# Optimization experiments

Hardware: AMD Instinct MI355X
Metric: run time of the kernel (lower is better)

## Reference

```python
import jax, jax.numpy as jnp
import numpy as np

B, T, V, E, H, C = 64, 512, 30000, 256, 512, 9


def setup_inputs() -> dict:
    key = jax.random.key(0)
    ks = jax.random.split(key, 12)
    s = 0.05
    x = jax.random.randint(ks[0], (B, T), 0, V, dtype=jnp.int32)
    seq_len = jax.random.randint(ks[1], (B,), T // 2, T + 1, dtype=jnp.int32)
    y = jax.random.randint(ks[2], (B, T), 0, C, dtype=jnp.int32)
    emb = jax.random.normal(ks[3], (V, E), jnp.float32) * s
    def lstm_p(k):
        k1, k2, k3 = jax.random.split(k, 3)
        return (jax.random.normal(k1, (4 * H, E), jnp.float32) * s,
                jax.random.normal(k2, (4 * H, H), jnp.float32) * s,
                jax.random.normal(k3, (4 * H,), jnp.float32) * s)
    Wih_f, Whh_f, b_f = lstm_p(ks[4])
    Wih_b, Whh_b, b_b = lstm_p(ks[5])
    Wfc = jax.random.normal(ks[6], (C, 2 * H), jnp.float32) * s
    start_t = jax.random.normal(ks[7], (C,), jnp.float32) * 0.1
    end_t = jax.random.normal(ks[8], (C,), jnp.float32) * 0.1
    trans = jax.random.normal(ks[9], (C, C), jnp.float32) * 0.1
    return dict(x=x, seq_len=seq_len, y=y, emb=emb, Wih_f=Wih_f, Whh_f=Whh_f,
                b_f=b_f, Wih_b=Wih_b, Whh_b=Whh_b, b_b=b_b, Wfc=Wfc,
                start_t=start_t, end_t=end_t, trans=trans)


def _lstm_dir(xt, mt, Wih, Whh, b, reverse):
    # xt: [T,B,E], mt: [T,B,1] bool. State frozen at padded steps (= packed-seq semantics).
    h0 = jnp.zeros((xt.shape[1], Whh.shape[1]), xt.dtype)
    def step(carry, inp):
        h, c = carry
        x_t, m_t = inp
        g = x_t @ Wih.T + h @ Whh.T + b
        i, f, gg, o = jnp.split(g, 4, axis=-1)  # torch gate order i,f,g,o
        c_new = jax.nn.sigmoid(f) * c + jax.nn.sigmoid(i) * jnp.tanh(gg)
        h_new = jax.nn.sigmoid(o) * jnp.tanh(c_new)
        return (jnp.where(m_t, h_new, h), jnp.where(m_t, c_new, c)), h_new
    _, hs = jax.lax.scan(step, (h0, h0), (xt, mt), reverse=reverse)
    return hs  # [T,B,H]


def reference(x, seq_len, y, emb, Wih_f, Whh_f, b_f, Wih_b, Whh_b, b_b, Wfc,
              start_t, end_t, trans):
    mask = jnp.arange(T)[None, :] < seq_len[:, None]  # [B,T]
    xt = emb[x].transpose(1, 0, 2)                    # [T,B,E]
    mt = mask.T[:, :, None]
    hf = _lstm_dir(xt, mt, Wih_f, Whh_f, b_f, False)
    hb = _lstm_dir(xt, mt, Wih_b, Whh_b, b_b, True)
    out = jnp.concatenate([hf, hb], -1).transpose(1, 0, 2)  # [B,T,2H]
    out = out * mask[:, :, None]                             # pad_packed zeros
    emis = jax.nn.log_softmax(out @ Wfc.T, axis=-1)          # [B,T,C]
    maskf = mask.astype(emis.dtype)
    # --- CRF numerator (gold-path score) ---
    em_sc = jnp.take_along_axis(emis, y[..., None], -1)[..., 0] * maskf
    tr_sc = trans[y[:, :-1], y[:, 1:]] * maskf[:, 1:]
    last_tag = jnp.take_along_axis(y, (seq_len - 1)[:, None], 1)[:, 0]
    num = start_t[y[:, 0]] + em_sc.sum(-1) + tr_sc.sum(-1) + end_t[last_tag]
    # --- CRF denominator (log partition, forward algorithm) ---
    score0 = start_t[None, :] + emis[:, 0]  # [B,C]
    def step(score, inp):
        em_t, m_t = inp  # [B,C], [B]
        nxt = jax.scipy.special.logsumexp(
            score[:, :, None] + trans[None] + em_t[:, None, :], axis=1)
        return jnp.where(m_t[:, None], nxt, score), None
    score, _ = jax.lax.scan(step, score0,
                            (emis.transpose(1, 0, 2)[1:], mask.T[1:]))
    den = jax.scipy.special.logsumexp(score + end_t[None, :], axis=1)
    return -(num - den).sum()  # -sum log-likelihood
```

## Files before the change

### kernel.cpp

```cpp
#include <hip/hip_runtime.h>
#include <hip/hip_bf16.h>


using short8 = __attribute__((ext_vector_type(8))) short;
using f32x4  = __attribute__((ext_vector_type(4))) float;
using i32x4  = __attribute__((ext_vector_type(4))) int;

#define TT 512
#define BB 64

__device__ __forceinline__ unsigned short f2bf(float f) {
  unsigned int u = __builtin_bit_cast(unsigned int, f);
  u += 0x7FFFu + ((u >> 16) & 1u);
  return (unsigned short)(u >> 16);
}
__device__ __forceinline__ float bf2f(short s) {
  unsigned int u = ((unsigned int)(unsigned short)s) << 16;
  return __builtin_bit_cast(float, u);
}
__device__ __forceinline__ float fast_rcp(float x) { return __builtin_amdgcn_rcpf(x); }
__device__ __forceinline__ float sigmoid_f(float x) { return fast_rcp(1.f + __expf(-x)); }
__device__ __forceinline__ float tanh_f(float x) {
  float e = __expf(-2.f * fabsf(x));
  float r = (1.f - e) * fast_rcp(1.f + e);
  return copysignf(r, x);
}
#define SEL4(i, a0, a1, a2, a3) ((i)==0?(a0):((i)==1?(a1):((i)==2?(a2):(a3))))

__device__ __forceinline__ i32x4 load16_sc(const void* p) {
  i32x4 r;
  asm volatile("global_load_dwordx4 %0, %1, off sc0 sc1" : "=v"(r) : "v"(p));
  return r;
}
__device__ __forceinline__ i32x4 load16_sc_wait(const void* p) {
  i32x4 r;
  asm volatile("global_load_dwordx4 %0, %1, off sc0 sc1\n\ts_waitcnt vmcnt(0)"
               : "=v"(r) : "v"(p) : "memory");
  return r;
}
__device__ __forceinline__ void store16_sc(void* p, i32x4 v) {
  asm volatile("global_store_dwordx4 %0, %1, off sc0 sc1" :: "v"(p), "v"(v) : "memory");
}
#define WAITV(n) do { asm volatile("s_waitcnt vmcnt(" #n ")" ::: "memory"); \
                      __builtin_amdgcn_sched_barrier(0); } while (0)

__global__ void pack_weights(const float* __restrict__ Wih_f, const float* __restrict__ Whh_f,
                             const float* __restrict__ Wih_b, const float* __restrict__ Whh_b,
                             const float* __restrict__ Wfc,
                             short* __restrict__ WpackX, short* __restrict__ WpackH,
                             short* __restrict__ WfcPack) {
  const int bid = blockIdx.x;
  const int d = bid & 1, sl = bid >> 1;
  const float* Wih = d ? Wih_b : Wih_f;
  const float* Whh = d ? Whh_b : Whh_f;
  for (int idx = threadIdx.x; idx < 64 * 256; idx += 256) {
    int n = idx >> 8, k = idx & 255;
    int g = n & 3, jq = (n >> 2) & 3, tj = (n >> 4) & 1, nt = n >> 5;
    int r = g * 512 + sl * 16 + nt * 8 + jq * 2 + tj;
    WpackX[((size_t)bid * 64 + n) * 256 + k] = (short)f2bf(Wih[(size_t)r * 256 + k]);
  }
  for (int idx = threadIdx.x; idx < 64 * 512; idx += 256) {
    int n = idx >> 9, k = idx & 511;
    int g = n & 3, jq = (n >> 2) & 3, tj = (n >> 4) & 1, nt = n >> 5;
    int r = g * 512 + sl * 16 + nt * 8 + jq * 2 + tj;
    WpackH[((size_t)bid * 64 + n) * 512 + k] = (short)f2bf(Whh[(size_t)r * 512 + k]);
  }
  if (bid == 0) {
    for (int idx = threadIdx.x; idx < 16 * 1024; idx += 256) {
      int c = idx >> 10, k = idx & 1023;
      WfcPack[idx] = (c < 9) ? (short)f2bf(Wfc[c * 1024 + k]) : (short)0;
    }
  }
}

__global__ void pack_x(const int* __restrict__ x, const float* __restrict__ emb,
                       short* __restrict__ xpack) {
  int gid = blockIdx.x * 256 + threadIdx.x;
  int lane = gid & 63;
  int kc = (gid >> 6) & 7;
  int mt = (gid >> 9) & 3;
  int t  = gid >> 11;
  int b  = mt * 16 + (lane & 15);
  int k0 = kc * 32 + (lane >> 4) * 8;
  int vid = x[b * TT + t];
  const float* e = emb + (size_t)vid * 256 + k0;
  short8 v;
#pragma unroll
  for (int i = 0; i < 8; ++i) v[i] = (short)f2bf(e[i]);
  *reinterpret_cast<short8*>(xpack + (size_t)gid * 8) = v;
}

__global__ void init_state(int* __restrict__ flags) {
  flags[threadIdx.x] = 0;
}

__launch_bounds__(256, 1)
__global__ void lstm_step_kernel(const short8* __restrict__ xpack,
                                 const short* __restrict__ WpackX,
                                 const short* __restrict__ WpackH,
                                 short* __restrict__ hexch,
                                 int* __restrict__ flags,
                                 const float* __restrict__ b_f,
                                 const float* __restrict__ b_b,
                                 const int* __restrict__ seq_len) {
  const int bid = blockIdx.x;
  const int d = bid & 1;
  const int sl = bid >> 1;
  const int tid = threadIdx.x;
  const int wv = tid >> 6;
  const int lane = tid & 63;
  const int l15 = lane & 15;
  const int lhi = lane >> 4;
  const int q = lane & 3;
  const int jq = l15 >> 2;
  const int mtb = wv & 1;
  const int nt = wv >> 1;
  const int nbase = nt * 32;
  const int ubase = sl * 16 + nt * 8;
  const int kc_w  = ubase >> 5;
  const int lhi_c = (ubase >> 3) & 3;

  short8 bfx[2][8];
#pragma unroll
  for (int tj = 0; tj < 2; ++tj)
#pragma unroll
    for (int kc = 0; kc < 8; ++kc)
      bfx[tj][kc] = *reinterpret_cast<const short8*>(
          WpackX + ((size_t)bid * 64 + nbase + tj * 16 + l15) * 256 + kc * 32 + lhi * 8);
  short8 bfh[2][16];
#pragma unroll
  for (int tj = 0; tj < 2; ++tj)
#pragma unroll
    for (int kc = 0; kc < 16; ++kc)
      bfh[tj][kc] = *reinterpret_cast<const short8*>(
          WpackH + ((size_t)bid * 64 + nbase + tj * 16 + l15) * 512 + kc * 32 + lhi * 8);

  const float* bias = d ? b_b : b_f;
  float bi[2], bfg[2], bgg[2], bog[2];
#pragma unroll
  for (int tj = 0; tj < 2; ++tj) {
    int jg = ubase + jq * 2 + tj;
    bi[tj]  = bias[jg];
    bfg[tj] = bias[512 + jg];
    bgg[tj] = bias[1024 + jg];
    bog[tj] = bias[1536 + jg];
  }
  int Lr[2];
#pragma unroll
  for (int ti = 0; ti < 2; ++ti)
    Lr[ti] = seq_len[mtb * 32 + ti * 16 + lhi * 4 + q];
  float cst[2][2] = {{0.f, 0.f}, {0.f, 0.f}};
  float hst[2][2] = {{0.f, 0.f}, {0.f, 0.f}};

  int* fl_grp  = flags + (d * 2 + mtb) * 64;
  int* fl_mine = fl_grp + (sl * 2 + nt);
  const int* fl_quad = fl_grp + (lane & 15) * 4;

  for (int s = 0; s < TT; ++s) {
    const int t = d ? (TT - 1 - s) : s;
    f32x4 acc[2][2];
#pragma unroll
    for (int ti = 0; ti < 2; ++ti)
#pragma unroll
      for (int tj = 0; tj < 2; ++tj) acc[ti][tj] = (f32x4){0.f, 0.f, 0.f, 0.f};

    const short8* xp = xpack + (size_t)t * 2048;
#pragma unroll
    for (int kc = 0; kc < 8; ++kc) {
      short8 af[2];
#pragma unroll
      for (int ti = 0; ti < 2; ++ti)
        af[ti] = xp[((mtb * 2 + ti) * 8 + kc) * 64 + lane];
#pragma unroll
      for (int ti = 0; ti < 2; ++ti)
#pragma unroll
        for (int tj = 0; tj < 2; ++tj)
          acc[ti][tj] = __builtin_amdgcn_mfma_f32_16x16x32_bf16(af[ti], bfx[tj][kc], acc[ti][tj], 0, 0, 0);
    }

    if (s > 0) {
      {
        int vtries = 0;
        while (true) {
          i32x4 f = load16_sc_wait(fl_quad);
          bool ok = (f[0] >= s) & (f[1] >= s) & (f[2] >= s) & (f[3] >= s);
          if (__all(ok)) break;
          __builtin_amdgcn_s_sleep(1);
          if (++vtries > (1 << 18)) break;
        }
      }
      __builtin_amdgcn_sched_barrier(0);

      const int tprev = d ? (t + 1) : (t - 1);
      const i32x4* hp16 = (const i32x4*)(hexch + ((size_t)d * TT + tprev) * 32768);
      i32x4 hbuf[32];
#pragma unroll
      for (int kc = 0; kc < 16; ++kc)
#pragma unroll
        for (int ti = 0; ti < 2; ++ti)
          hbuf[kc * 2 + ti] =
              load16_sc(hp16 + ((mtb * 16 + kc) * 2 + ti) * 64 + lane);
      WAITV(16);
#pragma unroll
      for (int kc = 0; kc < 8; ++kc)
#pragma unroll
        for (int ti = 0; ti < 2; ++ti) {
          short8 a = __builtin_bit_cast(short8, hbuf[kc * 2 + ti]);
#pragma unroll
          for (int tj = 0; tj < 2; ++tj)
            acc[ti][tj] = __builtin_amdgcn_mfma_f32_16x16x32_bf16(a, bfh[tj][kc], acc[ti][tj], 0, 0, 0);
        }
      WAITV(0);
#pragma unroll
      for (int kc = 8; kc < 16; ++kc)
#pragma unroll
        for (int ti = 0; ti < 2; ++ti) {
          short8 a = __builtin_bit_cast(short8, hbuf[kc * 2 + ti]);
#pragma unroll
          for (int tj = 0; tj < 2; ++tj)
            acc[ti][tj] = __builtin_amdgcn_mfma_f32_16x16x32_bf16(a, bfh[tj][kc], acc[ti][tj], 0, 0, 0);
        }
    }

    i32x4* hx16 = (i32x4*)(hexch + ((size_t)d * TT + t) * 32768);
#pragma unroll
    for (int ti = 0; ti < 2; ++ti) {
      bool m = (t < Lr[ti]);
      unsigned short hnb[2];
#pragma unroll
      for (int tj = 0; tj < 2; ++tj) {
        f32x4 A = acc[ti][tj];
        float a0 = A[0], a1 = A[1], a2 = A[2], a3 = A[3];
        float e10 = __shfl_xor(a0, 1, 64), e11 = __shfl_xor(a1, 1, 64),
              e12 = __shfl_xor(a2, 1, 64), e13 = __shfl_xor(a3, 1, 64);
        float e20 = __shfl_xor(a0, 2, 64), e21 = __shfl_xor(a1, 2, 64),
              e22 = __shfl_xor(a2, 2, 64), e23 = __shfl_xor(a3, 2, 64);
        float e30 = __shfl_xor(a0, 3, 64), e31 = __shfl_xor(a1, 3, 64),
              e32 = __shfl_xor(a2, 3, 64), e33 = __shfl_xor(a3, 3, 64);
        float g0 = SEL4(q, a0, a1, a2, a3);
        float g1 = SEL4(q, e10, e11, e12, e13);
        float g2 = SEL4(q, e20, e21, e22, e23);
        float g3 = SEL4(q, e30, e31, e32, e33);
        float gi = SEL4(q,     g0, g1, g2, g3) + bi[tj];
        float gf = SEL4(q ^ 1, g0, g1, g2, g3) + bfg[tj];
        float gg = SEL4(q ^ 2, g0, g1, g2, g3) + bgg[tj];
        float go = SEL4(q ^ 3, g0, g1, g2, g3) + bog[tj];
        float si = sigmoid_f(gi), sf = sigmoid_f(gf), so = sigmoid_f(go);
        float ct = sf * cst[ti][tj] + si * tanh_f(gg);
        float ht = so * tanh_f(ct);
        float cn = m ? ct : cst[ti][tj];
        float hn = m ? ht : hst[ti][tj];
        cst[ti][tj] = cn;
        hst[ti][tj] = hn;
        hnb[tj] = f2bf(hn);
      }
      unsigned int up = ((unsigned int)hnb[1] << 16) | hnb[0];
      unsigned int p1 = __shfl_xor(up, 4, 64), p2 = __shfl_xor(up, 8, 64),
                   p3 = __shfl_xor(up, 12, 64);
      if (jq == 0) {
        i32x4 packp = {(int)up, (int)p1, (int)p2, (int)p3};
        store16_sc(hx16 + ((mtb * 16 + kc_w) * 2 + ti) * 64 + lhi_c * 16 + lhi * 4 + q,
                   packp);
      }
    }

    if (lane == 0) {
      int sv = s + 1;
      asm volatile("s_waitcnt vmcnt(0)\n\t"
                   "global_store_dword %0, %1, off sc0 sc1"
                   :: "v"(fl_mine), "v"(sv) : "memory");
    }
  }
}

__launch_bounds__(256)
__global__ void emis_kernel(const short* __restrict__ hexch,
                            const short* __restrict__ WfcPack,
                            float* __restrict__ logits) {
  __shared__ short wfc[16 * 1032];
  const int tid = threadIdx.x;
  for (int idx = tid; idx < 2048; idx += 256) {
    int n = idx >> 7, c8 = idx & 127;
    short8 v = *reinterpret_cast<const short8*>(WfcPack + n * 1024 + c8 * 8);
    *reinterpret_cast<short8*>(&wfc[n * 1032 + c8 * 8]) = v;
  }
  __syncthreads();
  const int wv = tid >> 6, lane = tid & 63;
  const int l15 = lane & 15, lhi = lane >> 4;
  const i32x4* hx = (const i32x4*)hexch;
#pragma unroll
  for (int mt2 = 0; mt2 < 2; ++mt2) {
    int m = (blockIdx.x * 4 + wv) * 2 + mt2;
    int r0 = m * 16;
    int t   = r0 >> 6;
    int mtb = (r0 >> 5) & 1;
    int ti  = (r0 >> 4) & 1;
    f32x4 acc = (f32x4){0.f, 0.f, 0.f, 0.f};
#pragma unroll
    for (int kc = 0; kc < 32; ++kc) {
      int dd  = kc >> 4;
      int kcf = kc & 15;
      short8 a = __builtin_bit_cast(short8,
          hx[((size_t)dd * TT + t) * 4096 + ((mtb * 16 + kcf) * 2 + ti) * 64
             + lhi * 16 + l15]);
      short8 b = *reinterpret_cast<const short8*>(&wfc[l15 * 1032 + kc * 32 + lhi * 8]);
      acc = __builtin_amdgcn_mfma_f32_16x16x32_bf16(a, b, acc, 0, 0, 0);
    }
    int c = l15;
    if (c < 9) {
#pragma unroll
      for (int reg = 0; reg < 4; ++reg) {
        int rr = r0 + lhi * 4 + reg;
        int b = rr & 63, tt = rr >> 6;
        logits[((size_t)b * TT + tt) * 9 + c] = acc[reg];
      }
    }
  }
}

__global__ void crf_kernel(const float* __restrict__ logits, const int* __restrict__ y,
                           const int* __restrict__ seq_len, const float* __restrict__ start_t,
                           const float* __restrict__ end_t, const float* __restrict__ trans,
                           float* __restrict__ partials) {
  const int b = blockIdx.x;
  const int lane = threadIdx.x;
  const float* lg = logits + (size_t)b * TT * 9;
  const int* yb = y + b * TT;
  const int L = seq_len[b];

  float acc = 0.f;
  for (int t = lane; t < TT; t += 64) {
    if (t < L) {
      float mx = lg[t * 9];
      for (int c = 1; c < 9; ++c) mx = fmaxf(mx, lg[t * 9 + c]);
      float se = 0.f;
      for (int c = 0; c < 9; ++c) se += __expf(lg[t * 9 + c] - mx);
      float lse = mx + __logf(se);
      int yt = yb[t];
      acc += lg[t * 9 + yt] - lse;
      if (t >= 1) acc += trans[yb[t - 1] * 9 + yt];
    }
  }
#pragma unroll
  for (int off = 32; off >= 1; off >>= 1) acc += __shfl_down(acc, off, 64);

  const int c = (lane < 9) ? lane : 0;
  float score;
  {
    float mx = lg[0];
    for (int cc = 1; cc < 9; ++cc) mx = fmaxf(mx, lg[cc]);
    float se = 0.f;
    for (int cc = 0; cc < 9; ++cc) se += __expf(lg[cc] - mx);
    score = start_t[c] + lg[c] - (mx + __logf(se));
  }
  float tr[9];
#pragma unroll
  for (int cc = 0; cc < 9; ++cc) tr[cc] = trans[cc * 9 + c];
  for (int t = 1; t < L; ++t) {
    const float* lt = lg + t * 9;
    float mx2 = lt[0];
    for (int cc = 1; cc < 9; ++cc) mx2 = fmaxf(mx2, lt[cc]);
    float se2 = 0.f;
    for (int cc = 0; cc < 9; ++cc) se2 += __expf(lt[cc] - mx2);
    float em = lt[c] - (mx2 + __logf(se2));
    float vv[9];
    float mx = -1e30f;
#pragma unroll
    for (int cc = 0; cc < 9; ++cc) {
      float sp = __shfl(score, cc, 64);
      vv[cc] = sp + tr[cc];
      mx = fmaxf(mx, vv[cc]);
    }
    float se = 0.f;
#pragma unroll
    for (int cc = 0; cc < 9; ++cc) se += __expf(vv[cc] - mx);
    score = mx + __logf(se) + em;
  }
  float val = (lane < 9) ? (score + end_t[lane]) : -1e30f;
  float mm = val;
#pragma unroll
  for (int off = 1; off < 64; off <<= 1) mm = fmaxf(mm, __shfl_xor(mm, off, 64));
  float se = (lane < 9) ? __expf(val - mm) : 0.f;
#pragma unroll
  for (int off = 1; off < 64; off <<= 1) se += __shfl_xor(se, off, 64);
  float den = mm + __logf(se);
  if (lane == 0) {
    float num = acc + start_t[yb[0]] + end_t[yb[L - 1]];
    partials[b] = num - den;
  }
}

__global__ void finalize_kernel(const float* __restrict__ partials, float* __restrict__ out) {
  int l = threadIdx.x;
  float v = partials[l];
#pragma unroll
  for (int off = 32; off >= 1; off >>= 1) v += __shfl_down(v, off, 64);
  if (l == 0) out[0] = -v;
}

extern "C" void kernel_launch(void* const* d_in, const int* in_sizes, int n_in,
                              void* d_out, int out_size, void* d_ws, size_t ws_size,
                              hipStream_t stream) {
  const int*   x     = (const int*)d_in[0];
  const int*   seqln = (const int*)d_in[1];
  const int*   y     = (const int*)d_in[2];
  const float* emb   = (const float*)d_in[3];
  const float* Wih_f = (const float*)d_in[4];
  const float* Whh_f = (const float*)d_in[5];
  const float* b_f   = (const float*)d_in[6];
  const float* Wih_b = (const float*)d_in[7];
  const float* Whh_b = (const float*)d_in[8];
  const float* b_b   = (const float*)d_in[9];
  const float* Wfc   = (const float*)d_in[10];
  const float* st    = (const float*)d_in[11];
  const float* en    = (const float*)d_in[12];
  const float* trans = (const float*)d_in[13];
  float* out = (float*)d_out;

  char* ws = (char*)d_ws;
  short* WpackX   = (short*)(ws + 0);
  short* WpackH   = (short*)(ws + 2097152);
  short* WfcPack  = (short*)(ws + 6291456);
  short* xpack    = (short*)(ws + 6324224);
  int*   flags    = (int*)  (ws + 23101440);
  float* partials = (float*)(ws + 23102464);
  float* logits   = (float*)(ws + 23102720);
  short* hexch    = (short*)(ws + 24282368);

  pack_weights<<<64, 256, 0, stream>>>(Wih_f, Whh_f, Wih_b, Whh_b, Wfc,
                                       WpackX, WpackH, WfcPack);
  pack_x<<<4096, 256, 0, stream>>>(x, emb, xpack);
  init_state<<<1, 256, 0, stream>>>(flags);
  lstm_step_kernel<<<64, 256, 0, stream>>>((const short8*)xpack, WpackX, WpackH,
                                           hexch, flags, b_f, b_b, seqln);
  emis_kernel<<<256, 256, 0, stream>>>(hexch, WfcPack, logits);
  crf_kernel<<<64, 64, 0, stream>>>(logits, y, seqln, st, en, trans, partials);
  finalize_kernel<<<1, 64, 0, stream>>>(partials, out);
}
```

Before: 3.853 ms.

## Swap MFMA operand roles so gates land in one lane, drop gate shuffles

Transposes the recurrent GEMM so the weight tile is the A operand and the activations are B. With the packed weight row order permuted, each lane's accumulator then holds all four gates (i,f,g,o) for one unit. This removes the twelve cross-lane shuffles and the select chains per tile in the LSTM cell epilogue, along with the shuffles used to gather h for a 16-byte store. In exchange, each lane writes its h pair with a 4-byte store instead of a quarter of lanes issuing 16-byte stores, so the serial critical path gets more store instructions.

```diff
diff --git a/kernel.cpp b/kernel.cpp
--- a/kernel.cpp
+++ b/kernel.cpp
@@ -25,7 +25,6 @@
   float r = (1.f - e) * fast_rcp(1.f + e);
   return copysignf(r, x);
 }
-#define SEL4(i, a0, a1, a2, a3) ((i)==0?(a0):((i)==1?(a1):((i)==2?(a2):(a3))))
 
 __device__ __forceinline__ i32x4 load16_sc(const void* p) {
   i32x4 r;
@@ -38,8 +37,8 @@
                : "=v"(r) : "v"(p) : "memory");
   return r;
 }
-__device__ __forceinline__ void store16_sc(void* p, i32x4 v) {
-  asm volatile("global_store_dwordx4 %0, %1, off sc0 sc1" :: "v"(p), "v"(v) : "memory");
+__device__ __forceinline__ void store4_sc(void* p, unsigned int v) {
+  asm volatile("global_store_dword %0, %1, off sc0 sc1" :: "v"(p), "v"(v) : "memory");
 }
 #define WAITV(n) do { asm volatile("s_waitcnt vmcnt(" #n ")" ::: "memory"); \
                       __builtin_amdgcn_sched_barrier(0); } while (0)
@@ -55,14 +54,14 @@
   const float* Whh = d ? Whh_b : Whh_f;
   for (int idx = threadIdx.x; idx < 64 * 256; idx += 256) {
     int n = idx >> 8, k = idx & 255;
-    int g = n & 3, jq = (n >> 2) & 3, tj = (n >> 4) & 1, nt = n >> 5;
-    int r = g * 512 + sl * 16 + nt * 8 + jq * 2 + tj;
+    int nt = n >> 5, mi = (n >> 4) & 1, u = (n >> 2) & 3, g = n & 3;
+    int r = g * 512 + sl * 16 + nt * 8 + 2 * u + mi;
     WpackX[((size_t)bid * 64 + n) * 256 + k] = (short)f2bf(Wih[(size_t)r * 256 + k]);
   }
   for (int idx = threadIdx.x; idx < 64 * 512; idx += 256) {
     int n = idx >> 9, k = idx & 511;
-    int g = n & 3, jq = (n >> 2) & 3, tj = (n >> 4) & 1, nt = n >> 5;
-    int r = g * 512 + sl * 16 + nt * 8 + jq * 2 + tj;
+    int nt = n >> 5, mi = (n >> 4) & 1, u = (n >> 2) & 3, g = n & 3;
+    int r = g * 512 + sl * 16 + nt * 8 + 2 * u + mi;
     WpackH[((size_t)bid * 64 + n) * 512 + k] = (short)f2bf(Whh[(size_t)r * 512 + k]);
   }
   if (bid == 0) {
@@ -111,10 +110,9 @@
   const int lane = tid & 63;
   const int l15 = lane & 15;
   const int lhi = lane >> 4;
-  const int q = lane & 3;
-  const int jq = l15 >> 2;
   const int mtb = wv & 1;
   const int nt = wv >> 1;
+  const int mbase = mtb * 32;
   const int nbase = nt * 32;
   const int ubase = sl * 16 + nt * 8;
   const int kc_w  = ubase >> 5;
@@ -122,33 +120,31 @@
 
   short8 bfx[2][8];
 #pragma unroll
-  for (int tj = 0; tj < 2; ++tj)
+  for (int mi = 0; mi < 2; ++mi)
 #pragma unroll
     for (int kc = 0; kc < 8; ++kc)
-      bfx[tj][kc] = *reinterpret_cast<const short8*>(
-          WpackX + ((size_t)bid * 64 + nbase + tj * 16 + l15) * 256 + kc * 32 + lhi * 8);
+      bfx[mi][kc] = *reinterpret_cast<const short8*>(
+          WpackX + ((size_t)bid * 64 + nbase + mi * 16 + l15) * 256 + kc * 32 + lhi * 8);
   short8 bfh[2][16];
 #pragma unroll
-  for (int tj = 0; tj < 2; ++tj)
+  for (int mi = 0; mi < 2; ++mi)
 #pragma unroll
     for (int kc = 0; kc < 16; ++kc)
-      bfh[tj][kc] = *reinterpret_cast<const short8*>(
-          WpackH + ((size_t)bid * 64 + nbase + tj * 16 + l15) * 512 + kc * 32 + lhi * 8);
+      bfh[mi][kc] = *reinterpret_cast<const short8*>(
+          WpackH + ((size_t)bid * 64 + nbase + mi * 16 + l15) * 512 + kc * 32 + lhi * 8);
 
   const float* bias = d ? b_b : b_f;
-  float bi[2], bfg[2], bgg[2], bog[2];
-#pragma unroll
-  for (int tj = 0; tj < 2; ++tj) {
-    int jg = ubase + jq * 2 + tj;
-    bi[tj]  = bias[jg];
-    bfg[tj] = bias[512 + jg];
-    bgg[tj] = bias[1024 + jg];
-    bog[tj] = bias[1536 + jg];
+  float b4[2][4];
+#pragma unroll
+  for (int mi = 0; mi < 2; ++mi) {
+    int jg = ubase + 2 * lhi + mi;
+#pragma unroll
+    for (int g = 0; g < 4; ++g) b4[mi][g] = bias[g * 512 + jg];
   }
   int Lr[2];
 #pragma unroll
-  for (int ti = 0; ti < 2; ++ti)
-    Lr[ti] = seq_len[mtb * 32 + ti * 16 + lhi * 4 + q];
+  for (int ni = 0; ni < 2; ++ni)
+    Lr[ni] = seq_len[mbase + ni * 16 + l15];
   float cst[2][2] = {{0.f, 0.f}, {0.f, 0.f}};
   float hst[2][2] = {{0.f, 0.f}, {0.f, 0.f}};
 
@@ -160,22 +156,22 @@
     const int t = d ? (TT - 1 - s) : s;
     f32x4 acc[2][2];
 #pragma unroll
-    for (int ti = 0; ti < 2; ++ti)
-#pragma unroll
-      for (int tj = 0; tj < 2; ++tj) acc[ti][tj] = (f32x4){0.f, 0.f, 0.f, 0.f};
+    for (int mi = 0; mi < 2; ++mi)
+#pragma unroll
+      for (int ni = 0; ni < 2; ++ni) acc[mi][ni] = (f32x4){0.f, 0.f, 0.f, 0.f};
 
     const short8* xp = xpack + (size_t)t * 2048;
 #pragma unroll
     for (int kc = 0; kc < 8; ++kc) {
-      short8 af[2];
-#pragma unroll
-      for (int ti = 0; ti < 2; ++ti)
-        af[ti] = xp[((mtb * 2 + ti) * 8 + kc) * 64 + lane];
-#pragma unroll
-      for (int ti = 0; ti < 2; ++ti)
-#pragma unroll
-        for (int tj = 0; tj < 2; ++tj)
-          acc[ti][tj] = __builtin_amdgcn_mfma_f32_16x16x32_bf16(af[ti], bfx[tj][kc], acc[ti][tj], 0, 0, 0);
+      short8 bf[2];
+#pragma unroll
+      for (int ni = 0; ni < 2; ++ni)
+        bf[ni] = xp[((mtb * 2 + ni) * 8 + kc) * 64 + lane];
+#pragma unroll
+      for (int mi = 0; mi < 2; ++mi)
+#pragma unroll
+        for (int ni = 0; ni < 2; ++ni)
+          acc[mi][ni] = __builtin_amdgcn_mfma_f32_16x16x32_bf16(bfx[mi][kc], bf[ni], acc[mi][ni], 0, 0, 0);
     }
 
     if (s > 0) {
@@ -197,71 +193,57 @@
 #pragma unroll
       for (int kc = 0; kc < 16; ++kc)
 #pragma unroll
-        for (int ti = 0; ti < 2; ++ti)
-          hbuf[kc * 2 + ti] =
-              load16_sc(hp16 + ((mtb * 16 + kc) * 2 + ti) * 64 + lane);
+        for (int ni = 0; ni < 2; ++ni)
+          hbuf[kc * 2 + ni] =
+              load16_sc(hp16 + ((mtb * 16 + kc) * 2 + ni) * 64 + lane);
       WAITV(16);
 #pragma unroll
       for (int kc = 0; kc < 8; ++kc)
 #pragma unroll
-        for (int ti = 0; ti < 2; ++ti) {
-          short8 a = __builtin_bit_cast(short8, hbuf[kc * 2 + ti]);
-#pragma unroll
-          for (int tj = 0; tj < 2; ++tj)
-            acc[ti][tj] = __builtin_amdgcn_mfma_f32_16x16x32_bf16(a, bfh[tj][kc], acc[ti][tj], 0, 0, 0);
+        for (int ni = 0; ni < 2; ++ni) {
+          short8 b = __builtin_bit_cast(short8, hbuf[kc * 2 + ni]);
+#pragma unroll
+          for (int mi = 0; mi < 2; ++mi)
+            acc[mi][ni] = __builtin_amdgcn_mfma_f32_16x16x32_bf16(bfh[mi][kc], b, acc[mi][ni], 0, 0, 0);
         }
       WAITV(0);
 #pragma unroll
       for (int kc = 8; kc < 16; ++kc)
 #pragma unroll
-        for (int ti = 0; ti < 2; ++ti) {
-          short8 a = __builtin_bit_cast(short8, hbuf[kc * 2 + ti]);
-#pragma unroll
-          for (int tj = 0; tj < 2; ++tj)
-            acc[ti][tj] = __builtin_amdgcn_mfma_f32_16x16x32_bf16(a, bfh[tj][kc], acc[ti][tj], 0, 0, 0);
+        for (int ni = 0; ni < 2; ++ni) {
+          short8 b = __builtin_bit_cast(short8, hbuf[kc * 2 + ni]);
+#pragma unroll
+          for (int mi = 0; mi < 2; ++mi)
+            acc[mi][ni] = __builtin_amdgcn_mfma_f32_16x16x32_bf16(bfh[mi][kc], b, acc[mi][ni], 0, 0, 0);
         }
     }
 
-    i32x4* hx16 = (i32x4*)(hexch + ((size_t)d * TT + t) * 32768);
-#pragma unroll
-    for (int ti = 0; ti < 2; ++ti) {
-      bool m = (t < Lr[ti]);
+    short* hx = hexch + ((size_t)d * TT + t) * 32768;
+#pragma unroll
+    for (int ni = 0; ni < 2; ++ni) {
+      const bool m = (t < Lr[ni]);
       unsigned short hnb[2];
 #pragma unroll
-      for (int tj = 0; tj < 2; ++tj) {
-        f32x4 A = acc[ti][tj];
-        float a0 = A[0], a1 = A[1], a2 = A[2], a3 = A[3];
-        float e10 = __shfl_xor(a0, 1, 64), e11 = __shfl_xor(a1, 1, 64),
-              e12 = __shfl_xor(a2, 1, 64), e13 = __shfl_xor(a3, 1, 64);
-        float e20 = __shfl_xor(a0, 2, 64), e21 = __shfl_xor(a1, 2, 64),
-              e22 = __shfl_xor(a2, 2, 64), e23 = __shfl_xor(a3, 2, 64);
-        float e30 = __shfl_xor(a0, 3, 64), e31 = __shfl_xor(a1, 3, 64),
-              e32 = __shfl_xor(a2, 3, 64), e33 = __shfl_xor(a3, 3, 64);
-        float g0 = SEL4(q, a0, a1, a2, a3);
-        float g1 = SEL4(q, e10, e11, e12, e13);
-        float g2 = SEL4(q, e20, e21, e22, e23);
-        float g3 = SEL4(q, e30, e31, e32, e33);
-        float gi = SEL4(q,     g0, g1, g2, g3) + bi[tj];
-        float gf = SEL4(q ^ 1, g0, g1, g2, g3) + bfg[tj];
-        float gg = SEL4(q ^ 2, g0, g1, g2, g3) + bgg[tj];
-        float go = SEL4(q ^ 3, g0, g1, g2, g3) + bog[tj];
+      for (int mi = 0; mi < 2; ++mi) {
+        f32x4 A = acc[mi][ni];
+        float gi = A[0] + b4[mi][0];
+        float gf = A[1] + b4[mi][1];
+        float gg = A[2] + b4[mi][2];
+        float go = A[3] + b4[mi][3];
         float si = sigmoid_f(gi), sf = sigmoid_f(gf), so = sigmoid_f(go);
-        float ct = sf * cst[ti][tj] + si * tanh_f(gg);
+        float ct = sf * cst[mi][ni] + si * tanh_f(gg);
         float ht = so * tanh_f(ct);
-        float cn = m ? ct : cst[ti][tj];
-        float hn = m ? ht : hst[ti][tj];
-        cst[ti][tj] = cn;
-        hst[ti][tj] = hn;
-        hnb[tj] = f2bf(hn);
+        float cn = m ? ct : cst[mi][ni];
+        float hn = m ? ht : hst[mi][ni];
+        cst[mi][ni] = cn;
+        hst[mi][ni] = hn;
+        hnb[mi] = f2bf(hn);
       }
       unsigned int up = ((unsigned int)hnb[1] << 16) | hnb[0];
-      unsigned int p1 = __shfl_xor(up, 4, 64), p2 = __shfl_xor(up, 8, 64),
-                   p3 = __shfl_xor(up, 12, 64);
-      if (jq == 0) {
-        i32x4 packp = {(int)up, (int)p1, (int)p2, (int)p3};
-        store16_sc(hx16 + ((mtb * 16 + kc_w) * 2 + ti) * 64 + lhi_c * 16 + lhi * 4 + q,
-                   packp);
-      }
+      store4_sc((char*)hx
+                    + (size_t)(((mtb * 16 + kc_w) * 2 + ni) * 64 + lhi_c * 16 + l15) * 16
+                    + lhi * 4,
+                up);
     }
 
     if (lane == 0) {
```

Measured after the change: 3.242 ms, median of 2. 1.19x faster.
